# Kernel optimization log

Measured on AMD Instinct MI355X. Metric: run time of the kernel, lower is better.

The kernel has to match this reference:

```python
import jax, jax.numpy as jnp
import numpy as np

# Physics config (DPhysConfig defaults for the tracked robot)
MASS = 40.0        # robot mass [kg]
GRAV = 9.8         # gravity magnitude
STIFF = 1000.0     # terrain stiffness
DAMP = 100.0       # terrain damping
OMEGA_MAX = 2.0    # angular velocity clamp
DT = 0.01          # integration step [s]
LY = 0.6           # robot width (track separation)
RES = 0.1          # grid resolution [m/cell]


def skew(v):
    # v: (..., 3) -> (..., 3, 3)
    z = jnp.zeros_like(v[..., 0])
    return jnp.stack([
        jnp.stack([z, -v[..., 2], v[..., 1]], -1),
        jnp.stack([v[..., 2], z, -v[..., 0]], -1),
        jnp.stack([-v[..., 1], v[..., 0], z], -1)], -2)


def normalized(x, eps=1e-6):
    return x / jnp.clip(jnp.linalg.norm(x, axis=-1, keepdims=True), eps)


def bilinear(grid, xq, yq):
    # grid: (B, H, W) over [-H*RES/2, H*RES/2] x [-W*RES/2, W*RES/2]; xq, yq: (B, N)
    B, H, W = grid.shape
    u = jnp.clip((xq + H * RES / 2) / RES, 0.0, H - 1.001)
    v = jnp.clip((yq + W * RES / 2) / RES, 0.0, W - 1.001)
    u0 = jnp.floor(u).astype(jnp.int32)
    v0 = jnp.floor(v).astype(jnp.int32)
    du, dv = u - u0, v - v0
    b = jnp.arange(B)[:, None]
    g00 = grid[b, u0, v0]
    g10 = grid[b, u0 + 1, v0]
    g01 = grid[b, u0, v0 + 1]
    g11 = grid[b, u0 + 1, v0 + 1]
    return (g00 * (1 - du) * (1 - dv) + g10 * du * (1 - dv)
            + g01 * (1 - du) * dv + g11 * du * dv)


def inertia_inv(points, mass):
    # points: (N, 3) body-frame point masses -> inverse inertia (3, 3)
    mp = mass / points.shape[0]
    x, y, z = points[:, 0], points[:, 1], points[:, 2]
    Ixx = (mp * (y ** 2 + z ** 2)).sum()
    Iyy = (mp * (x ** 2 + z ** 2)).sum()
    Izz = (mp * (x ** 2 + y ** 2)).sum()
    Ixy = -(mp * x * y).sum()
    Ixz = -(mp * x * z).sum()
    Iyz = -(mp * y * z).sum()
    I = jnp.stack([jnp.stack([Ixx, Ixy, Ixz]),
                   jnp.stack([Ixy, Iyy, Iyz]),
                   jnp.stack([Ixz, Iyz, Izz])])
    return jnp.linalg.inv(I)


def _forward(z_grid, friction, controls, robot_points, x0, xd0, R0, omega0):
    dtype = z_grid.dtype
    I_inv = inertia_inv(robot_points, MASS)          # (3,3), joints fixed -> constant
    gx = jnp.gradient(z_grid, axis=1) / RES          # dz/dx on grid
    gy = jnp.gradient(z_grid, axis=2) / RES          # dz/dy on grid
    maskL = (robot_points[:, 1] < 0).astype(dtype)   # (N,) left track points
    maskR = 1.0 - maskL                              # right track points
    F_grav = MASS * GRAV * jnp.array([0.0, 0.0, -1.0], dtype=dtype)
    clamp = MASS * GRAV

    def dynamics(state, ctrl):
        x, xd, R, omega = state
        # world-frame body points: x_points @ R^T + x
        pts = jnp.einsum('nj,bkj->bnk', robot_points, R) + x[:, None]      # (B,N,3)
        xd_pts = xd[:, None] + jnp.cross(omega[:, None, :], pts - x[:, None], axis=-1)
        px, py = pts[..., 0], pts[..., 1]
        z = bilinear(z_grid, px, py)[..., None]                            # (B,N,1)
        nrm = normalized(jnp.stack([-bilinear(gx, px, py),
                                    -bilinear(gy, px, py),
                                    jnp.ones_like(px)], -1))               # (B,N,3)
        fr = bilinear(friction, px, py)[..., None]                         # (B,N,1)
        dh = pts[..., 2:3] - z
        in_c = jax.nn.sigmoid(-10.0 * dh)
        xd_n = jnp.sum(xd_pts * nrm, -1, keepdims=True)
        F_r = -(STIFF * dh + DAMP * xd_n) * nrm
        F_r = jnp.clip(F_r * in_c / jnp.sum(in_c, 1, keepdims=True), -clamp, clamp)
        thrust = normalized(R[..., 0])                                     # (B,3) first column
        Nmag = jnp.linalg.norm(F_r, axis=2)                                # (B,N)
        v, w = ctrl[:, 0], ctrl[:, 1]
        vL = (v - w * LY / 2)[:, None, None]
        vR = (v + w * LY / 2)[:, None, None]
        cmd = (maskL[None, :, None] * vL + maskR[None, :, None] * vR) * thrust[:, None, :]
        slip = fr * (cmd - xd_pts)
        slip_tau = slip - jnp.sum(slip * nrm, -1, keepdims=True) * nrm
        F_f = jnp.clip(Nmag[..., None] * slip_tau, -clamp, clamp)
        torque = jnp.sum(jnp.cross(pts - x[:, None], F_r + F_f, axis=-1), axis=1)
        omega_d = jnp.clip(torque @ I_inv.T, -OMEGA_MAX, OMEGA_MAX)
        xdd = (F_grav[None] + F_r.sum(1) + F_f.sum(1)) / MASS
        return xdd, omega_d

    def rot_step(R, omega, eps=1e-6):
        # Rodrigues' formula
        Ox = skew(omega)
        th = jnp.linalg.norm(omega, axis=-1)[:, None, None]
        Oxn = Ox / jnp.clip(th, eps)
        I3 = jnp.eye(3, dtype=R.dtype)
        return R @ (I3 + Oxn * jnp.sin(th * DT) + (Oxn @ Oxn) * (1 - jnp.cos(th * DT)))

    def step(state, ctrl):
        x, xd, R, omega = state
        xdd, omega_d = dynamics(state, ctrl)
        xd = xd + xdd * DT          # semi-implicit Euler, as in update_state
        x = x + xd * DT
        omega = omega + omega_d * DT
        R = rot_step(R, omega)
        return (x, xd, R, omega), x

    _, Xs = jax.lax.scan(step, (x0, xd0, R0, omega0), jnp.swapaxes(controls, 0, 1))
    return jnp.swapaxes(Xs, 0, 1)   # (B, T, 3) trajectory positions


def setup_inputs() -> dict:
    key = jax.random.key(0)
    ks = jax.random.split(key, 5)
    B, T, N, H, W = 64, 500, 128, 256, 256
    z_grid = jax.random.uniform(ks[0], (B, H, W), dtype=jnp.float32) * 0.2
    friction = jax.random.uniform(ks[1], (B, H, W), dtype=jnp.float32)
    controls = jax.random.normal(ks[2], (B, T, 2), dtype=jnp.float32) * jnp.array([1.0, 0.5], jnp.float32)
    robot_points = (jax.random.uniform(ks[3], (N, 3), dtype=jnp.float32) - 0.5) \
        * jnp.array([1.0, 0.6, 0.2], jnp.float32)
    x0 = jax.random.normal(ks[4], (B, 3), dtype=jnp.float32) * 0.1 + jnp.array([0.0, 0.0, 0.3], jnp.float32)
    xd0 = jnp.zeros((B, 3), jnp.float32)
    R0 = jnp.tile(jnp.eye(3, dtype=jnp.float32), (B, 1, 1))
    omega0 = jnp.zeros((B, 3), jnp.float32)
    return {"z_grid": z_grid, "friction": friction, "controls": controls,
            "robot_points": robot_points, "x0": x0, "xd0": xd0, "R0": R0, "omega0": omega0}


def reference(z_grid, friction, controls, robot_points, x0, xd0, R0, omega0):
    return _forward(z_grid, friction, controls, robot_points, x0, xd0, R0, omega0)
```

## Files before the change

kernel.cpp:

```cpp
#include <hip/hip_runtime.h>
#include <math.h>

#define GH 256
#define GW 256

typedef float f4 __attribute__((ext_vector_type(4), aligned(4)));
typedef float f2 __attribute__((ext_vector_type(2), aligned(4)));
typedef float f4l __attribute__((ext_vector_type(4)));

template<int CTRL, int RMASK>
__device__ __forceinline__ float dpp_add(float v) {
    int r = __builtin_amdgcn_update_dpp(0, __builtin_bit_cast(int, v), CTRL, RMASK, 0xF, true);
    return v + __builtin_bit_cast(float, r);
}
template<int CTRL, int RMASK>
__device__ __forceinline__ float dpp_max(float v) {
    int r = __builtin_amdgcn_update_dpp(0, __builtin_bit_cast(int, v), CTRL, RMASK, 0xF, true);
    return fmaxf(v, __builtin_bit_cast(float, r));
}

__device__ __forceinline__ float wave_sum63(float v) {
    v = dpp_add<0xB1, 0xF>(v);
    v = dpp_add<0x4E, 0xF>(v);
    v = dpp_add<0x141, 0xF>(v);
    v = dpp_add<0x140, 0xF>(v);
    v = dpp_add<0x142, 0xA>(v);
    v = dpp_add<0x143, 0xC>(v);
    return v;
}
__device__ __forceinline__ float wave_max63(float v) {
    v = dpp_max<0xB1, 0xF>(v);
    v = dpp_max<0x4E, 0xF>(v);
    v = dpp_max<0x141, 0xF>(v);
    v = dpp_max<0x140, 0xF>(v);
    v = dpp_max<0x142, 0xA>(v);
    v = dpp_max<0x143, 0xC>(v);
    return v;
}
__device__ __forceinline__ float rl63(float v) {
    return __builtin_bit_cast(float, __builtin_amdgcn_readlane(__builtin_bit_cast(int, v), 63));
}

__device__ __forceinline__ float frcp(float x)  { return __builtin_amdgcn_rcpf(x); }
__device__ __forceinline__ float frsq(float x)  { return __builtin_amdgcn_rsqf(x); }
__device__ __forceinline__ float fexp2(float x) { return __builtin_amdgcn_exp2f(x); }

__global__ __launch_bounds__(128) void dphys_kernel(
    const float* __restrict__ z_grid,
    const float* __restrict__ friction,
    const float* __restrict__ controls,
    const float* __restrict__ robot_points,
    const float* __restrict__ x0,
    const float* __restrict__ xd0,
    const float* __restrict__ R0,
    const float* __restrict__ omega0,
    float* __restrict__ out,
    int T)
{
    const int b = blockIdx.x;
    const int tid = threadIdx.x;
    const int wv = tid >> 6;
    __shared__ f4l ldsX[2][2][2];
    __shared__ f4l ldsY[2][2];

    const float* __restrict__ zg = z_grid + (size_t)b * (GH * GW);
    const float* __restrict__ fg = friction + (size_t)b * (GH * GW);
    const float* __restrict__ ct = controls + (size_t)b * (T * 2);
    float* __restrict__ ob = out + (size_t)b * (T * 3);

    const float ppx = robot_points[tid * 3 + 0];
    const float ppy = robot_points[tid * 3 + 1];
    const float ppz = robot_points[tid * 3 + 2];
    const bool isL = (ppy < 0.0f);

    float I6[6];
    I6[0] = ppy * ppy + ppz * ppz;
    I6[1] = ppx * ppx + ppz * ppz;
    I6[2] = ppx * ppx + ppy * ppy;
    I6[3] = ppx * ppy;
    I6[4] = ppx * ppz;
    I6[5] = ppy * ppz;
    #pragma unroll
    for (int k = 0; k < 6; ++k) I6[k] = rl63(wave_sum63(I6[k]));
    if ((tid & 63) == 63) {
        f4l t0; t0.x = I6[0]; t0.y = I6[1]; t0.z = I6[2]; t0.w = I6[3];
        f4l t1; t1.x = I6[4]; t1.y = I6[5]; t1.z = 0.f; t1.w = 0.f;
        ldsY[wv][0] = t0; ldsY[wv][1] = t1;
    }
    __syncthreads();
    {
        f4l o0 = ldsY[wv ^ 1][0], o1 = ldsY[wv ^ 1][1];
        I6[0] += o0.x; I6[1] += o0.y; I6[2] += o0.z;
        I6[3] += o0.w; I6[4] += o1.x; I6[5] += o1.y;
    }
    const float mp = 0.3125f;
    {
        double a = mp * I6[0], bb = mp * I6[1], c = mp * I6[2];
        double d = -(mp * I6[3]), e = -(mp * I6[4]), f = -(mp * I6[5]);
        double C00 = bb * c - f * f, C01 = e * f - d * c, C02 = d * f - bb * e;
        double C11 = a * c - e * e, C12 = d * e - a * f, C22 = a * bb - d * d;
        double idet = 1.0 / (a * C00 + d * C01 + e * C02);
        I6[0] = (float)(C00 * idet); I6[1] = (float)(C11 * idet); I6[2] = (float)(C22 * idet);
        I6[3] = (float)(C01 * idet); I6[4] = (float)(C02 * idet); I6[5] = (float)(C12 * idet);
    }
    const float i00 = I6[0], i11 = I6[1], i22 = I6[2];
    const float i01 = I6[3], i02 = I6[4], i12 = I6[5];

    float X0 = x0[b * 3 + 0], X1 = x0[b * 3 + 1], X2 = x0[b * 3 + 2];
    float V0 = xd0[b * 3 + 0], V1 = xd0[b * 3 + 1], V2 = xd0[b * 3 + 2];
    float W0 = omega0[b * 3 + 0], W1 = omega0[b * 3 + 1], W2 = omega0[b * 3 + 2];
    float R00 = R0[b * 9 + 0], R01 = R0[b * 9 + 1], R02 = R0[b * 9 + 2];
    float R10 = R0[b * 9 + 3], R11 = R0[b * 9 + 4], R12 = R0[b * 9 + 5];
    float R20 = R0[b * 9 + 6], R21 = R0[b * 9 + 7], R22 = R0[b * 9 + 8];

    for (int t = 0; t < T; ++t) {
        const int par = t & 1;
        f2 cc = *(const f2*)(ct + t * 2);

        float rx = R00 * ppx + R01 * ppy + R02 * ppz;
        float ry = R10 * ppx + R11 * ppy + R12 * ppz;
        float rz = R20 * ppx + R21 * ppy + R22 * ppz;
        float Px = rx + X0, Py = ry + X1, Pz = rz + X2;
        float l0 = Px - X0, l1 = Py - X1, l2 = Pz - X2;
        float u = (Px + 12.8f) * 10.0f;
        u = fminf(fmaxf(u, 0.0f), 254.999f);
        float vvq = (Py + 12.8f) * 10.0f;
        vvq = fminf(fmaxf(vvq, 0.0f), 254.999f);
        int u0 = (int)u, v0 = (int)vvq;
        bool interior = (u0 >= 1) & (u0 <= 253) & (v0 >= 1) & (v0 <= 253);
        bool fast = __all(interior);

        float zz, fr, gxs, gys;
        float du = u - (float)u0, dv = vvq - (float)v0;
        float w00 = (1.0f - du) * (1.0f - dv);
        float w10 = du * (1.0f - dv);
        float w01 = (1.0f - du) * dv;
        float w11 = du * dv;

        float cv = cc.x, cw = cc.y;
        float half = (cw * 0.6f) * 0.5f;
        float vLs = cv - half, vRs = cv + half;
        float rtn = frsq(R00 * R00 + R10 * R10 + R20 * R20);
        float th0 = R00 * rtn, th1 = R10 * rtn, th2 = R20 * rtn;
        float xp0 = V0 + (W1 * l2 - W2 * l1);
        float xp1 = V1 + (W2 * l0 - W0 * l2);
        float xp2 = V2 + (W0 * l1 - W1 * l0);
        float cmd = isL ? vLs : vRs;
        float ct0 = cmd * th0 - xp0;
        float ct1 = cmd * th1 - xp1;
        float ct2 = cmd * th2 - xp2;

        if (fast) {
            int base = (u0 - 1) * GW + (v0 - 1);
            f4 P0 = *(const f4*)(zg + base);
            f4 P1 = *(const f4*)(zg + base + GW);
            f4 P2 = *(const f4*)(zg + base + 2 * GW);
            f4 P3 = *(const f4*)(zg + base + 3 * GW);
            int fb = u0 * GW + v0;
            f2 F0 = *(const f2*)(fg + fb);
            f2 F1 = *(const f2*)(fg + fb + GW);
            zz = P1.y * w00 + P2.y * w10 + P1.z * w01 + P2.z * w11;
            fr = F0.x * w00 + F1.x * w10 + F0.y * w01 + F1.y * w11;
            float gx00 = (P2.y - P0.y) * 5.0f;
            float gx10 = (P3.y - P1.y) * 5.0f;
            float gx01 = (P2.z - P0.z) * 5.0f;
            float gx11 = (P3.z - P1.z) * 5.0f;
            float gy00 = (P1.z - P1.x) * 5.0f;
            float gy10 = (P2.z - P2.x) * 5.0f;
            float gy01 = (P1.w - P1.y) * 5.0f;
            float gy11 = (P2.w - P2.y) * 5.0f;
            gxs = gx00 * w00 + gx10 * w10 + gx01 * w01 + gx11 * w11;
            gys = gy00 * w00 + gy10 * w10 + gy01 * w01 + gy11 * w11;
        } else {
            int basei = u0 * GW + v0;
            zz = zg[basei] * w00 + zg[basei + GW] * w10 + zg[basei + 1] * w01 + zg[basei + GW + 1] * w11;
            fr = fg[basei] * w00 + fg[basei + GW] * w10 + fg[basei + 1] * w01 + fg[basei + GW + 1] * w11;
            float gx[2][2], gy[2][2];
            #pragma unroll
            for (int ii = 0; ii < 2; ++ii) {
                int i = u0 + ii;
                int ipu = (i < GH - 1) ? i + 1 : i;
                int imu = (i > 0) ? i - 1 : i;
                float scu = (ipu - imu == 2) ? 0.5f : 1.0f;
                #pragma unroll
                for (int jj = 0; jj < 2; ++jj) {
                    int j = v0 + jj;
                    int jpv = (j < GW - 1) ? j + 1 : j;
                    int jmv = (j > 0) ? j - 1 : j;
                    float scv = (jpv - jmv == 2) ? 0.5f : 1.0f;
                    gx[ii][jj] = ((zg[ipu * GW + j] - zg[imu * GW + j]) * scu) * 10.0f;
                    gy[ii][jj] = ((zg[i * GW + jpv] - zg[i * GW + jmv]) * scv) * 10.0f;
                }
            }
            gxs = gx[0][0] * w00 + gx[1][0] * w10 + gx[0][1] * w01 + gx[1][1] * w11;
            gys = gy[0][0] * w00 + gy[1][0] * w10 + gy[0][1] * w01 + gy[1][1] * w11;
        }

        float rn = frsq(gxs * gxs + gys * gys + 1.0f);
        float nx = -gxs * rn, ny = -gys * rn, nzc = rn;
        float dh = Pz - zz;
        float ex = fexp2(dh * 14.426950408889634f);
        float ic = frcp(1.0f + ex);
        float xdn = xp0 * nx + xp1 * ny + xp2 * nzc;

        float mag = -(1000.0f * dh + 100.0f * xdn);
        float mic = mag * ic;
        float m_abs = fabsf(mic);
        float sl0 = fr * ct0, sl1 = fr * ct1, sl2 = fr * ct2;
        float sdn = sl0 * nx + sl1 * ny + sl2 * nzc;
        float st0 = sl0 - sdn * nx;
        float st1 = sl1 - sdn * ny;
        float st2 = sl2 - sdn * nzc;
        float g0 = mic * nx  + m_abs * st0;
        float g1 = mic * ny  + m_abs * st1;
        float g2 = mic * nzc + m_abs * st2;
        float q0 = l1 * g2 - l2 * g1;
        float q1 = l2 * g0 - l0 * g2;
        float q2 = l0 * g1 - l1 * g0;
        float stm = fmaxf(fmaxf(fabsf(st0), fabsf(st1)), fabsf(st2));
        float worst = fmaxf(stm, 1.0f) * m_abs;

        float d_ic = wave_sum63(ic);
        float d_g0 = wave_sum63(g0), d_g1 = wave_sum63(g1), d_g2 = wave_sum63(g2);
        float d_q0 = wave_sum63(q0), d_q1 = wave_sum63(q1), d_q2 = wave_sum63(q2);
        float d_rw = wave_max63(worst);
        if ((tid & 63) == 63) {
            f4l h0; h0.x = d_g0; h0.y = d_g1; h0.z = d_g2; h0.w = d_q0;
            f4l h1; h1.x = d_q1; h1.y = d_q2; h1.z = d_ic; h1.w = d_rw;
            ldsX[par][wv][0] = h0; ldsX[par][wv][1] = h1;
        }
        float o_ic = rl63(d_ic);
        float o_g0 = rl63(d_g0), o_g1 = rl63(d_g1), o_g2 = rl63(d_g2);
        float o_q0 = rl63(d_q0), o_q1 = rl63(d_q1), o_q2 = rl63(d_q2);
        float o_rw = rl63(d_rw);
        __syncthreads();
        f4l e0 = ldsX[par][wv ^ 1][0], e1 = ldsX[par][wv ^ 1][1];
        float sic = o_ic + e1.z;
        float rwm = fmaxf(o_rw, e1.w);
        float rsic = frcp(sic);

        float FT0, FT1, FT2, TQ0, TQ1, TQ2;
        if (rwm <= 391.0f * sic) {
            FT0 = (o_g0 + e0.x) * rsic;
            FT1 = (o_g1 + e0.y) * rsic;
            FT2 = (o_g2 + e0.z) * rsic;
            TQ0 = (o_q0 + e0.w) * rsic;
            TQ1 = (o_q1 + e1.x) * rsic;
            TQ2 = (o_q2 + e1.y) * rsic;
        } else {
            float s = mic * rsic;
            float Fr0 = fminf(fmaxf(s * nx,  -392.0f), 392.0f);
            float Fr1 = fminf(fmaxf(s * ny,  -392.0f), 392.0f);
            float Fr2 = fminf(fmaxf(s * nzc, -392.0f), 392.0f);
            float Nm = __builtin_amdgcn_sqrtf(Fr0 * Fr0 + Fr1 * Fr1 + Fr2 * Fr2);
            float Ff0 = fminf(fmaxf(Nm * st0, -392.0f), 392.0f);
            float Ff1 = fminf(fmaxf(Nm * st1, -392.0f), 392.0f);
            float Ff2 = fminf(fmaxf(Nm * st2, -392.0f), 392.0f);
            float S0 = Fr0 + Ff0, S1 = Fr1 + Ff1, S2 = Fr2 + Ff2;
            float U0 = l1 * S2 - l2 * S1;
            float U1 = l2 * S0 - l0 * S2;
            float U2 = l0 * S1 - l1 * S0;
            float dS0 = wave_sum63(S0), dS1 = wave_sum63(S1), dS2 = wave_sum63(S2);
            float dU0 = wave_sum63(U0), dU1 = wave_sum63(U1), dU2 = wave_sum63(U2);
            if ((tid & 63) == 63) {
                f4l h0; h0.x = dS0; h0.y = dS1; h0.z = dS2; h0.w = dU0;
                f4l h1; h1.x = dU1; h1.y = dU2; h1.z = 0.f; h1.w = 0.f;
                ldsY[wv][0] = h0; ldsY[wv][1] = h1;
            }
            __syncthreads();
            f4l c0 = ldsY[wv ^ 1][0], c1 = ldsY[wv ^ 1][1];
            FT0 = rl63(dS0) + c0.x; FT1 = rl63(dS1) + c0.y; FT2 = rl63(dS2) + c0.z;
            TQ0 = rl63(dU0) + c0.w; TQ1 = rl63(dU1) + c1.x; TQ2 = rl63(dU2) + c1.y;
        }

        float od0 = fminf(fmaxf(TQ0 * i00 + TQ1 * i01 + TQ2 * i02, -2.0f), 2.0f);
        float od1 = fminf(fmaxf(TQ0 * i01 + TQ1 * i11 + TQ2 * i12, -2.0f), 2.0f);
        float od2 = fminf(fmaxf(TQ0 * i02 + TQ1 * i12 + TQ2 * i22, -2.0f), 2.0f);

        V0 += (FT0 * 0.025f) * 0.01f;
        V1 += (FT1 * 0.025f) * 0.01f;
        V2 += ((-392.0f + FT2) * 0.025f) * 0.01f;
        X0 += V0 * 0.01f; X1 += V1 * 0.01f; X2 += V2 * 0.01f;
        W0 += od0 * 0.01f; W1 += od1 * 0.01f; W2 += od2 * 0.01f;

        if (tid == 0) {
            ob[t * 3 + 0] = X0;
            ob[t * 3 + 1] = X1;
            ob[t * 3 + 2] = X2;
        }

        float th2s = W0 * W0 + W1 * W1 + W2 * W2;
        float a2 = th2s * 1e-4f;
        float s1 = 0.01f - a2 * (0.01f / 6.0f);
        float c2 = 5e-5f - a2 * (1e-4f / 24.0f);
        float w01p = W0 * W1, w02p = W0 * W2, w12p = W1 * W2;
        float A00 = 1.0f - c2 * (W1 * W1 + W2 * W2);
        float A11 = 1.0f - c2 * (W0 * W0 + W2 * W2);
        float A22 = 1.0f - c2 * (W0 * W0 + W1 * W1);
        float A01 = c2 * w01p - s1 * W2;
        float A10 = c2 * w01p + s1 * W2;
        float A02 = c2 * w02p + s1 * W1;
        float A20 = c2 * w02p - s1 * W1;
        float A12 = c2 * w12p - s1 * W0;
        float A21 = c2 * w12p + s1 * W0;
        float N00 = R00 * A00 + R01 * A10 + R02 * A20;
        float N01 = R00 * A01 + R01 * A11 + R02 * A21;
        float N02 = R00 * A02 + R01 * A12 + R02 * A22;
        float N10 = R10 * A00 + R11 * A10 + R12 * A20;
        float N11 = R10 * A01 + R11 * A11 + R12 * A21;
        float N12 = R10 * A02 + R11 * A12 + R12 * A22;
        float N20 = R20 * A00 + R21 * A10 + R22 * A20;
        float N21 = R20 * A01 + R21 * A11 + R22 * A21;
        float N22 = R20 * A02 + R21 * A12 + R22 * A22;
        R00 = N00; R01 = N01; R02 = N02;
        R10 = N10; R11 = N11; R12 = N12;
        R20 = N20; R21 = N21; R22 = N22;
    }
}

extern "C" void kernel_launch(void* const* d_in, const int* in_sizes, int n_in,
                              void* d_out, int out_size, void* d_ws, size_t ws_size,
                              hipStream_t stream) {
    const float* z_grid       = (const float*)d_in[0];
    const float* friction     = (const float*)d_in[1];
    const float* controls     = (const float*)d_in[2];
    const float* robot_points = (const float*)d_in[3];
    const float* x0           = (const float*)d_in[4];
    const float* xd0          = (const float*)d_in[5];
    const float* R0           = (const float*)d_in[6];
    const float* omega0       = (const float*)d_in[7];
    int B = in_sizes[4] / 3;
    int T = in_sizes[2] / (B * 2);
    dphys_kernel<<<B, 128, 0, stream>>>(z_grid, friction, controls, robot_points,
                                        x0, xd0, R0, omega0, (float*)d_out, T);
}
```

Before: 554.9 us.

## Precompute interleaved height/gradient/friction texture in workspace for single-gather bilinear lookups

Adds a prep kernel that writes a float4 per grid cell holding height, x/y gradients and friction into the workspace. The main simulation kernel then does four float4 gathers and one vector bilinear blend per step, replacing separate height and friction loads, on-the-fly gradient stencils and the interior/boundary branch. The loop is also unrolled by two. This costs an extra launch and about 67 MB of workspace writes and reads, and the old kernel remains as a fallback when the workspace is too small.

```diff
diff --git a/kernel.cpp b/kernel.cpp
--- a/kernel.cpp
+++ b/kernel.cpp
@@ -18,7 +18,6 @@
     int r = __builtin_amdgcn_update_dpp(0, __builtin_bit_cast(int, v), CTRL, RMASK, 0xF, true);
     return fmaxf(v, __builtin_bit_cast(float, r));
 }
-
 __device__ __forceinline__ float wave_sum63(float v) {
     v = dpp_add<0xB1, 0xF>(v);
     v = dpp_add<0x4E, 0xF>(v);
@@ -40,12 +39,266 @@
 __device__ __forceinline__ float rl63(float v) {
     return __builtin_bit_cast(float, __builtin_amdgcn_readlane(__builtin_bit_cast(int, v), 63));
 }
-
 __device__ __forceinline__ float frcp(float x)  { return __builtin_amdgcn_rcpf(x); }
 __device__ __forceinline__ float frsq(float x)  { return __builtin_amdgcn_rsqf(x); }
 __device__ __forceinline__ float fexp2(float x) { return __builtin_amdgcn_exp2f(x); }
 
+__global__ __launch_bounds__(256) void prep_kernel(
+    const float* __restrict__ z_grid,
+    const float* __restrict__ friction,
+    f4* __restrict__ tex)
+{
+    const int j = threadIdx.x;
+    const int i = blockIdx.x;
+    const int b = blockIdx.y;
+    const float* __restrict__ z = z_grid + (size_t)b * (GH * GW);
+    int ipu = (i < GH - 1) ? i + 1 : i;
+    int imu = (i > 0) ? i - 1 : i;
+    int jpv = (j < GW - 1) ? j + 1 : j;
+    int jmv = (j > 0) ? j - 1 : j;
+    float scu = (ipu - imu == 2) ? 0.5f : 1.0f;
+    float scv = (jpv - jmv == 2) ? 0.5f : 1.0f;
+    float gx = ((z[ipu * GW + j] - z[imu * GW + j]) * scu) * 10.0f;
+    float gy = ((z[i * GW + jpv] - z[i * GW + jmv]) * scv) * 10.0f;
+    f4 o;
+    o.x = z[i * GW + j];
+    o.y = gx;
+    o.z = gy;
+    o.w = friction[(size_t)b * (GH * GW) + i * GW + j];
+    tex[(size_t)b * (GH * GW) + i * GW + j] = o;
+}
+
 __global__ __launch_bounds__(128) void dphys_kernel(
+    const f4* __restrict__ tex,
+    const float* __restrict__ controls,
+    const float* __restrict__ robot_points,
+    const float* __restrict__ x0,
+    const float* __restrict__ xd0,
+    const float* __restrict__ R0,
+    const float* __restrict__ omega0,
+    float* __restrict__ out,
+    int T)
+{
+    const int b = blockIdx.x;
+    const int tid = threadIdx.x;
+    const int wv = tid >> 6;
+    __shared__ f4l ldsX[2][2][2];
+    __shared__ f4l ldsY[2][2];
+
+    const f4* __restrict__ tb = tex + (size_t)b * (GH * GW);
+    const float* __restrict__ ct = controls + (size_t)b * (T * 2);
+    float* __restrict__ ob = out + (size_t)b * (T * 3);
+
+    const float ppx = robot_points[tid * 3 + 0];
+    const float ppy = robot_points[tid * 3 + 1];
+    const float ppz = robot_points[tid * 3 + 2];
+    const bool isL = (ppy < 0.0f);
+
+    float I6[6];
+    I6[0] = ppy * ppy + ppz * ppz;
+    I6[1] = ppx * ppx + ppz * ppz;
+    I6[2] = ppx * ppx + ppy * ppy;
+    I6[3] = ppx * ppy;
+    I6[4] = ppx * ppz;
+    I6[5] = ppy * ppz;
+    #pragma unroll
+    for (int k = 0; k < 6; ++k) I6[k] = rl63(wave_sum63(I6[k]));
+    if ((tid & 63) == 63) {
+        f4l t0; t0.x = I6[0]; t0.y = I6[1]; t0.z = I6[2]; t0.w = I6[3];
+        f4l t1; t1.x = I6[4]; t1.y = I6[5]; t1.z = 0.f; t1.w = 0.f;
+        ldsY[wv][0] = t0; ldsY[wv][1] = t1;
+    }
+    __syncthreads();
+    {
+        f4l o0 = ldsY[wv ^ 1][0], o1 = ldsY[wv ^ 1][1];
+        I6[0] += o0.x; I6[1] += o0.y; I6[2] += o0.z;
+        I6[3] += o0.w; I6[4] += o1.x; I6[5] += o1.y;
+    }
+    const float mp = 0.3125f;
+    {
+        double a = mp * I6[0], bb = mp * I6[1], c = mp * I6[2];
+        double d = -(mp * I6[3]), e = -(mp * I6[4]), f = -(mp * I6[5]);
+        double C00 = bb * c - f * f, C01 = e * f - d * c, C02 = d * f - bb * e;
+        double C11 = a * c - e * e, C12 = d * e - a * f, C22 = a * bb - d * d;
+        double idet = 1.0 / (a * C00 + d * C01 + e * C02);
+        I6[0] = (float)(C00 * idet); I6[1] = (float)(C11 * idet); I6[2] = (float)(C22 * idet);
+        I6[3] = (float)(C01 * idet); I6[4] = (float)(C02 * idet); I6[5] = (float)(C12 * idet);
+    }
+    const float i00 = I6[0], i11 = I6[1], i22 = I6[2];
+    const float i01 = I6[3], i02 = I6[4], i12 = I6[5];
+
+    float X0 = x0[b * 3 + 0], X1 = x0[b * 3 + 1], X2 = x0[b * 3 + 2];
+    float V0 = xd0[b * 3 + 0], V1 = xd0[b * 3 + 1], V2 = xd0[b * 3 + 2];
+    float W0 = omega0[b * 3 + 0], W1 = omega0[b * 3 + 1], W2 = omega0[b * 3 + 2];
+    float R00 = R0[b * 9 + 0], R01 = R0[b * 9 + 1], R02 = R0[b * 9 + 2];
+    float R10 = R0[b * 9 + 3], R11 = R0[b * 9 + 4], R12 = R0[b * 9 + 5];
+    float R20 = R0[b * 9 + 6], R21 = R0[b * 9 + 7], R22 = R0[b * 9 + 8];
+
+    #pragma unroll 2
+    for (int t = 0; t < T; ++t) {
+        const int par = t & 1;
+        f2 cc = *(const f2*)(ct + t * 2);
+
+        float rx = R00 * ppx + R01 * ppy + R02 * ppz;
+        float ry = R10 * ppx + R11 * ppy + R12 * ppz;
+        float rz = R20 * ppx + R21 * ppy + R22 * ppz;
+        float Px = rx + X0, Py = ry + X1, Pz = rz + X2;
+        float l0 = Px - X0, l1 = Py - X1, l2 = Pz - X2;
+        float u = (Px + 12.8f) * 10.0f;
+        u = fminf(fmaxf(u, 0.0f), 254.999f);
+        float vvq = (Py + 12.8f) * 10.0f;
+        vvq = fminf(fmaxf(vvq, 0.0f), 254.999f);
+        int u0 = (int)u, v0 = (int)vvq;
+        int idx = (u0 << 8) + v0;
+        f4 c00 = tb[idx];
+        f4 c01 = tb[idx + 1];
+        f4 c10 = tb[idx + GW];
+        f4 c11 = tb[idx + GW + 1];
+
+        float du = u - (float)u0, dv = vvq - (float)v0;
+        float w00 = (1.0f - du) * (1.0f - dv);
+        float w10 = du * (1.0f - dv);
+        float w01 = (1.0f - du) * dv;
+        float w11 = du * dv;
+        float cv = cc.x, cw = cc.y;
+        float half = (cw * 0.6f) * 0.5f;
+        float vLs = cv - half, vRs = cv + half;
+        float rtn = frsq(R00 * R00 + R10 * R10 + R20 * R20);
+        float th0 = R00 * rtn, th1 = R10 * rtn, th2 = R20 * rtn;
+        float xp0 = V0 + (W1 * l2 - W2 * l1);
+        float xp1 = V1 + (W2 * l0 - W0 * l2);
+        float xp2 = V2 + (W0 * l1 - W1 * l0);
+        float cmd = isL ? vLs : vRs;
+        float ct0 = cmd * th0 - xp0;
+        float ct1 = cmd * th1 - xp1;
+        float ct2 = cmd * th2 - xp2;
+
+        f4 cb = c00 * w00 + c10 * w10 + c01 * w01 + c11 * w11;
+        float zz = cb.x, gxs = cb.y, gys = cb.z, fr = cb.w;
+
+        float rn = frsq(gxs * gxs + gys * gys + 1.0f);
+        float nx = -gxs * rn, ny = -gys * rn, nzc = rn;
+        float dh = Pz - zz;
+        float ex = fexp2(dh * 14.426950408889634f);
+        float ic = frcp(1.0f + ex);
+        float xdn = xp0 * nx + xp1 * ny + xp2 * nzc;
+
+        float mag = -(1000.0f * dh + 100.0f * xdn);
+        float mic = mag * ic;
+        float m_abs = fabsf(mic);
+        float sl0 = fr * ct0, sl1 = fr * ct1, sl2 = fr * ct2;
+        float sdn = sl0 * nx + sl1 * ny + sl2 * nzc;
+        float st0 = sl0 - sdn * nx;
+        float st1 = sl1 - sdn * ny;
+        float st2 = sl2 - sdn * nzc;
+        float g0 = mic * nx  + m_abs * st0;
+        float g1 = mic * ny  + m_abs * st1;
+        float g2 = mic * nzc + m_abs * st2;
+        float q0 = l1 * g2 - l2 * g1;
+        float q1 = l2 * g0 - l0 * g2;
+        float q2 = l0 * g1 - l1 * g0;
+        float stm = fmaxf(fmaxf(fabsf(st0), fabsf(st1)), fabsf(st2));
+        float worst = fmaxf(stm, 1.0f) * m_abs;
+
+        float d_ic = wave_sum63(ic);
+        float d_g0 = wave_sum63(g0), d_g1 = wave_sum63(g1), d_g2 = wave_sum63(g2);
+        float d_q0 = wave_sum63(q0), d_q1 = wave_sum63(q1), d_q2 = wave_sum63(q2);
+        float d_rw = wave_max63(worst);
+        if ((tid & 63) == 63) {
+            f4l h0; h0.x = d_g0; h0.y = d_g1; h0.z = d_g2; h0.w = d_q0;
+            f4l h1; h1.x = d_q1; h1.y = d_q2; h1.z = d_ic; h1.w = d_rw;
+            ldsX[par][wv][0] = h0; ldsX[par][wv][1] = h1;
+        }
+        float o_ic = rl63(d_ic);
+        float o_g0 = rl63(d_g0), o_g1 = rl63(d_g1), o_g2 = rl63(d_g2);
+        float o_q0 = rl63(d_q0), o_q1 = rl63(d_q1), o_q2 = rl63(d_q2);
+        float o_rw = rl63(d_rw);
+        __syncthreads();
+        f4l e0 = ldsX[par][wv ^ 1][0], e1 = ldsX[par][wv ^ 1][1];
+        float sic = o_ic + e1.z;
+        float rwm = fmaxf(o_rw, e1.w);
+        float rsic = frcp(sic);
+
+        float FT0, FT1, FT2, TQ0, TQ1, TQ2;
+        if (rwm <= 391.0f * sic) {
+            FT0 = (o_g0 + e0.x) * rsic;
+            FT1 = (o_g1 + e0.y) * rsic;
+            FT2 = (o_g2 + e0.z) * rsic;
+            TQ0 = (o_q0 + e0.w) * rsic;
+            TQ1 = (o_q1 + e1.x) * rsic;
+            TQ2 = (o_q2 + e1.y) * rsic;
+        } else {
+            float s = mic * rsic;
+            float Fr0 = fminf(fmaxf(s * nx,  -392.0f), 392.0f);
+            float Fr1 = fminf(fmaxf(s * ny,  -392.0f), 392.0f);
+            float Fr2 = fminf(fmaxf(s * nzc, -392.0f), 392.0f);
+            float Nm = __builtin_amdgcn_sqrtf(Fr0 * Fr0 + Fr1 * Fr1 + Fr2 * Fr2);
+            float Ff0 = fminf(fmaxf(Nm * st0, -392.0f), 392.0f);
+            float Ff1 = fminf(fmaxf(Nm * st1, -392.0f), 392.0f);
+            float Ff2 = fminf(fmaxf(Nm * st2, -392.0f), 392.0f);
+            float S0 = Fr0 + Ff0, S1 = Fr1 + Ff1, S2 = Fr2 + Ff2;
+            float U0 = l1 * S2 - l2 * S1;
+            float U1 = l2 * S0 - l0 * S2;
+            float U2 = l0 * S1 - l1 * S0;
+            float dS0 = wave_sum63(S0), dS1 = wave_sum63(S1), dS2 = wave_sum63(S2);
+            float dU0 = wave_sum63(U0), dU1 = wave_sum63(U1), dU2 = wave_sum63(U2);
+            if ((tid & 63) == 63) {
+                f4l h0; h0.x = dS0; h0.y = dS1; h0.z = dS2; h0.w = dU0;
+                f4l h1; h1.x = dU1; h1.y = dU2; h1.z = 0.f; h1.w = 0.f;
+                ldsY[wv][0] = h0; ldsY[wv][1] = h1;
+            }
+            __syncthreads();
+            f4l c0 = ldsY[wv ^ 1][0], c1 = ldsY[wv ^ 1][1];
+            FT0 = rl63(dS0) + c0.x; FT1 = rl63(dS1) + c0.y; FT2 = rl63(dS2) + c0.z;
+            TQ0 = rl63(dU0) + c0.w; TQ1 = rl63(dU1) + c1.x; TQ2 = rl63(dU2) + c1.y;
+        }
+
+        float od0 = fminf(fmaxf(TQ0 * i00 + TQ1 * i01 + TQ2 * i02, -2.0f), 2.0f);
+        float od1 = fminf(fmaxf(TQ0 * i01 + TQ1 * i11 + TQ2 * i12, -2.0f), 2.0f);
+        float od2 = fminf(fmaxf(TQ0 * i02 + TQ1 * i12 + TQ2 * i22, -2.0f), 2.0f);
+
+        V0 += (FT0 * 0.025f) * 0.01f;
+        V1 += (FT1 * 0.025f) * 0.01f;
+        V2 += ((-392.0f + FT2) * 0.025f) * 0.01f;
+        X0 += V0 * 0.01f; X1 += V1 * 0.01f; X2 += V2 * 0.01f;
+        W0 += od0 * 0.01f; W1 += od1 * 0.01f; W2 += od2 * 0.01f;
+
+        if (tid == 0) {
+            ob[t * 3 + 0] = X0;
+            ob[t * 3 + 1] = X1;
+            ob[t * 3 + 2] = X2;
+        }
+
+        float th2s = W0 * W0 + W1 * W1 + W2 * W2;
+        float a2 = th2s * 1e-4f;
+        float s1 = 0.01f - a2 * (0.01f / 6.0f);
+        float c2 = 5e-5f - a2 * (1e-4f / 24.0f);
+        float w01p = W0 * W1, w02p = W0 * W2, w12p = W1 * W2;
+        float A00 = 1.0f - c2 * (W1 * W1 + W2 * W2);
+        float A11 = 1.0f - c2 * (W0 * W0 + W2 * W2);
+        float A22 = 1.0f - c2 * (W0 * W0 + W1 * W1);
+        float A01 = c2 * w01p - s1 * W2;
+        float A10 = c2 * w01p + s1 * W2;
+        float A02 = c2 * w02p + s1 * W1;
+        float A20 = c2 * w02p - s1 * W1;
+        float A12 = c2 * w12p - s1 * W0;
+        float A21 = c2 * w12p + s1 * W0;
+        float N00 = R00 * A00 + R01 * A10 + R02 * A20;
+        float N01 = R00 * A01 + R01 * A11 + R02 * A21;
+        float N02 = R00 * A02 + R01 * A12 + R02 * A22;
+        float N10 = R10 * A00 + R11 * A10 + R12 * A20;
+        float N11 = R10 * A01 + R11 * A11 + R12 * A21;
+        float N12 = R10 * A02 + R11 * A12 + R12 * A22;
+        float N20 = R20 * A00 + R21 * A10 + R22 * A20;
+        float N21 = R20 * A01 + R21 * A11 + R22 * A21;
+        float N22 = R20 * A02 + R21 * A12 + R22 * A22;
+        R00 = N00; R01 = N01; R02 = N02;
+        R10 = N10; R11 = N11; R12 = N12;
+        R20 = N20; R21 = N21; R22 = N22;
+    }
+}
+
+__global__ __launch_bounds__(128) void dphys_kernel_fb(
     const float* __restrict__ z_grid,
     const float* __restrict__ friction,
     const float* __restrict__ controls,
@@ -116,7 +369,6 @@
     for (int t = 0; t < T; ++t) {
         const int par = t & 1;
         f2 cc = *(const f2*)(ct + t * 2);
-
         float rx = R00 * ppx + R01 * ppy + R02 * ppz;
         float ry = R10 * ppx + R11 * ppy + R12 * ppz;
         float rz = R20 * ppx + R21 * ppy + R22 * ppz;
@@ -128,7 +380,7 @@
         vvq = fminf(fmaxf(vvq, 0.0f), 254.999f);
         int u0 = (int)u, v0 = (int)vvq;
         bool interior = (u0 >= 1) & (u0 <= 253) & (v0 >= 1) & (v0 <= 253);
-        bool fast = __all(interior);
+        bool fastp = __all(interior);
 
         float zz, fr, gxs, gys;
         float du = u - (float)u0, dv = vvq - (float)v0;
@@ -150,7 +402,7 @@
         float ct1 = cmd * th1 - xp1;
         float ct2 = cmd * th2 - xp2;
 
-        if (fast) {
+        if (fastp) {
             int base = (u0 - 1) * GW + (v0 - 1);
             f4 P0 = *(const f4*)(zg + base);
             f4 P1 = *(const f4*)(zg + base + GW);
@@ -331,6 +583,13 @@
     const float* omega0       = (const float*)d_in[7];
     int B = in_sizes[4] / 3;
     int T = in_sizes[2] / (B * 2);
-    dphys_kernel<<<B, 128, 0, stream>>>(z_grid, friction, controls, robot_points,
-                                        x0, xd0, R0, omega0, (float*)d_out, T);
-}
+    size_t need = (size_t)B * GH * GW * sizeof(float) * 4;
+    if (ws_size >= need) {
+        prep_kernel<<<dim3(GH, B), GW, 0, stream>>>(z_grid, friction, (f4*)d_ws);
+        dphys_kernel<<<B, 128, 0, stream>>>((const f4*)d_ws, controls, robot_points,
+                                            x0, xd0, R0, omega0, (float*)d_out, T);
+    } else {
+        dphys_kernel_fb<<<B, 128, 0, stream>>>(z_grid, friction, controls, robot_points,
+                                               x0, xd0, R0, omega0, (float*)d_out, T);
+    }
+}
```

Result: faster. 479.9 us (-13.5%).

## Precompute interleaved height/gradient/friction texture and simulate two batches per block

Applied to the files above, without the earlier changes.

Adds a prep kernel that packs height, the central-difference gradients and friction into one float4 per cell in the workspace. The main kernel then does four float4 gathers per point per step and handles two batch elements per 128-thread block, using paired f2 arithmetic so the two serial step chains interleave. This targets per-step gather latency and the latency-bound serial loop. In exchange it adds a full-grid preprocessing pass, 64 MB of workspace traffic, and halves the number of blocks. The old kernel is kept as a fallback when the workspace is too small.

```diff
diff --git a/kernel.cpp b/kernel.cpp
--- a/kernel.cpp
+++ b/kernel.cpp
@@ -18,7 +18,6 @@
     int r = __builtin_amdgcn_update_dpp(0, __builtin_bit_cast(int, v), CTRL, RMASK, 0xF, true);
     return fmaxf(v, __builtin_bit_cast(float, r));
 }
-
 __device__ __forceinline__ float wave_sum63(float v) {
     v = dpp_add<0xB1, 0xF>(v);
     v = dpp_add<0x4E, 0xF>(v);
@@ -40,12 +39,338 @@
 __device__ __forceinline__ float rl63(float v) {
     return __builtin_bit_cast(float, __builtin_amdgcn_readlane(__builtin_bit_cast(int, v), 63));
 }
-
 __device__ __forceinline__ float frcp(float x)  { return __builtin_amdgcn_rcpf(x); }
 __device__ __forceinline__ float frsq(float x)  { return __builtin_amdgcn_rsqf(x); }
 __device__ __forceinline__ float fexp2(float x) { return __builtin_amdgcn_exp2f(x); }
 
-__global__ __launch_bounds__(128) void dphys_kernel(
+__device__ __forceinline__ f2 pabs(f2 a)        { f2 r; r.x = fabsf(a.x); r.y = fabsf(a.y); return r; }
+__device__ __forceinline__ f2 pmaxv(f2 a, f2 b) { f2 r; r.x = fmaxf(a.x, b.x); r.y = fmaxf(a.y, b.y); return r; }
+__device__ __forceinline__ f2 pclamp(f2 a, float lo, float hi) {
+    f2 r; r.x = fminf(fmaxf(a.x, lo), hi); r.y = fminf(fmaxf(a.y, lo), hi); return r;
+}
+__device__ __forceinline__ f2 prsq(f2 a) { f2 r; r.x = frsq(a.x); r.y = frsq(a.y); return r; }
+
+__global__ __launch_bounds__(256) void prep_kernel(
+    const float* __restrict__ z_grid,
+    const float* __restrict__ friction,
+    f4* __restrict__ tex)
+{
+    const int j = threadIdx.x;
+    const int i = blockIdx.x;
+    const int b = blockIdx.y;
+    const float* __restrict__ z = z_grid + (size_t)b * (GH * GW);
+    int ipu = (i < GH - 1) ? i + 1 : i;
+    int imu = (i > 0) ? i - 1 : i;
+    int jpv = (j < GW - 1) ? j + 1 : j;
+    int jmv = (j > 0) ? j - 1 : j;
+    float scu = (ipu - imu == 2) ? 0.5f : 1.0f;
+    float scv = (jpv - jmv == 2) ? 0.5f : 1.0f;
+    float gx = ((z[ipu * GW + j] - z[imu * GW + j]) * scu) * 10.0f;
+    float gy = ((z[i * GW + jpv] - z[i * GW + jmv]) * scv) * 10.0f;
+    f4 o;
+    o.x = z[i * GW + j];
+    o.y = gx;
+    o.z = gy;
+    o.w = friction[(size_t)b * (GH * GW) + i * GW + j];
+    tex[(size_t)b * (GH * GW) + i * GW + j] = o;
+}
+
+__global__ __launch_bounds__(128, 1) void dphys_kernel2p(
+    const f4* __restrict__ tex,
+    const float* __restrict__ controls,
+    const float* __restrict__ robot_points,
+    const float* __restrict__ x0,
+    const float* __restrict__ xd0,
+    const float* __restrict__ R0,
+    const float* __restrict__ omega0,
+    float* __restrict__ out,
+    int T, int B)
+{
+    const int tid = threadIdx.x;
+    const int wv = tid >> 6;
+    __shared__ f4l ldsX[2][2][2][2];
+    __shared__ f4l ldsY[2][2][2];
+
+    int bA = blockIdx.x * 2;
+    int bB = bA + 1; if (bB >= B) bB = B - 1;
+
+    const f4* __restrict__ tbA = tex + (size_t)bA * (GH * GW);
+    const f4* __restrict__ tbB = tex + (size_t)bB * (GH * GW);
+    const float* __restrict__ ctA = controls + (size_t)bA * (T * 2);
+    const float* __restrict__ ctB = controls + (size_t)bB * (T * 2);
+    float* __restrict__ obA = out + (size_t)bA * (T * 3);
+    float* __restrict__ obB = out + (size_t)bB * (T * 3);
+
+    const float ppx = robot_points[tid * 3 + 0];
+    const float ppy = robot_points[tid * 3 + 1];
+    const float ppz = robot_points[tid * 3 + 2];
+    const bool isL = (ppy < 0.0f);
+
+    float I6[6];
+    I6[0] = ppy * ppy + ppz * ppz;
+    I6[1] = ppx * ppx + ppz * ppz;
+    I6[2] = ppx * ppx + ppy * ppy;
+    I6[3] = ppx * ppy;
+    I6[4] = ppx * ppz;
+    I6[5] = ppy * ppz;
+    #pragma unroll
+    for (int k = 0; k < 6; ++k) I6[k] = rl63(wave_sum63(I6[k]));
+    if ((tid & 63) == 63) {
+        f4l t0; t0.x = I6[0]; t0.y = I6[1]; t0.z = I6[2]; t0.w = I6[3];
+        f4l t1; t1.x = I6[4]; t1.y = I6[5]; t1.z = 0.f; t1.w = 0.f;
+        ldsY[0][wv][0] = t0; ldsY[0][wv][1] = t1;
+    }
+    __syncthreads();
+    {
+        f4l o0 = ldsY[0][wv ^ 1][0], o1 = ldsY[0][wv ^ 1][1];
+        I6[0] += o0.x; I6[1] += o0.y; I6[2] += o0.z;
+        I6[3] += o0.w; I6[4] += o1.x; I6[5] += o1.y;
+    }
+    const float mp = 0.3125f;
+    {
+        double a = mp * I6[0], bb = mp * I6[1], c = mp * I6[2];
+        double d = -(mp * I6[3]), e = -(mp * I6[4]), f = -(mp * I6[5]);
+        double C00 = bb * c - f * f, C01 = e * f - d * c, C02 = d * f - bb * e;
+        double C11 = a * c - e * e, C12 = d * e - a * f, C22 = a * bb - d * d;
+        double idet = 1.0 / (a * C00 + d * C01 + e * C02);
+        I6[0] = (float)(C00 * idet); I6[1] = (float)(C11 * idet); I6[2] = (float)(C22 * idet);
+        I6[3] = (float)(C01 * idet); I6[4] = (float)(C02 * idet); I6[5] = (float)(C12 * idet);
+    }
+    const float i00 = I6[0], i11 = I6[1], i22 = I6[2];
+    const float i01 = I6[3], i02 = I6[4], i12 = I6[5];
+
+    f2 X0, X1, X2, V0, V1, V2, W0, W1, W2;
+    f2 R00, R01, R02, R10, R11, R12, R20, R21, R22;
+    X0.x = x0[bA*3+0]; X0.y = x0[bB*3+0];
+    X1.x = x0[bA*3+1]; X1.y = x0[bB*3+1];
+    X2.x = x0[bA*3+2]; X2.y = x0[bB*3+2];
+    V0.x = xd0[bA*3+0]; V0.y = xd0[bB*3+0];
+    V1.x = xd0[bA*3+1]; V1.y = xd0[bB*3+1];
+    V2.x = xd0[bA*3+2]; V2.y = xd0[bB*3+2];
+    W0.x = omega0[bA*3+0]; W0.y = omega0[bB*3+0];
+    W1.x = omega0[bA*3+1]; W1.y = omega0[bB*3+1];
+    W2.x = omega0[bA*3+2]; W2.y = omega0[bB*3+2];
+    R00.x = R0[bA*9+0]; R00.y = R0[bB*9+0];
+    R01.x = R0[bA*9+1]; R01.y = R0[bB*9+1];
+    R02.x = R0[bA*9+2]; R02.y = R0[bB*9+2];
+    R10.x = R0[bA*9+3]; R10.y = R0[bB*9+3];
+    R11.x = R0[bA*9+4]; R11.y = R0[bB*9+4];
+    R12.x = R0[bA*9+5]; R12.y = R0[bB*9+5];
+    R20.x = R0[bA*9+6]; R20.y = R0[bB*9+6];
+    R21.x = R0[bA*9+7]; R21.y = R0[bB*9+7];
+    R22.x = R0[bA*9+8]; R22.y = R0[bB*9+8];
+
+    for (int t = 0; t < T; ++t) {
+        const int par = t & 1;
+        f2 ccA = *(const f2*)(ctA + t * 2);
+        f2 ccB = *(const f2*)(ctB + t * 2);
+        f2 cv; cv.x = ccA.x; cv.y = ccB.x;
+        f2 cw; cw.x = ccA.y; cw.y = ccB.y;
+
+        f2 rx = R00 * ppx + R01 * ppy + R02 * ppz;
+        f2 ry = R10 * ppx + R11 * ppy + R12 * ppz;
+        f2 rz = R20 * ppx + R21 * ppy + R22 * ppz;
+        f2 Px = rx + X0, Py = ry + X1, Pz = rz + X2;
+        f2 l0 = Px - X0, l1 = Py - X1, l2 = Pz - X2;
+        f2 u = pclamp((Px + 12.8f) * 10.0f, 0.0f, 254.999f);
+        f2 vq = pclamp((Py + 12.8f) * 10.0f, 0.0f, 254.999f);
+        int u0A = (int)u.x, u0B = (int)u.y;
+        int v0A = (int)vq.x, v0B = (int)vq.y;
+        f2 du; du.x = u.x - (float)u0A; du.y = u.y - (float)u0B;
+        f2 dv; dv.x = vq.x - (float)v0A; dv.y = vq.y - (float)v0B;
+        int idxA = (u0A << 8) + v0A;
+        int idxB = (u0B << 8) + v0B;
+        f4 a00 = tbA[idxA], a01 = tbA[idxA + 1], a10 = tbA[idxA + GW], a11 = tbA[idxA + GW + 1];
+        f4 b00 = tbB[idxB], b01 = tbB[idxB + 1], b10 = tbB[idxB + GW], b11 = tbB[idxB + GW + 1];
+
+        f2 half_ = (cw * 0.6f) * 0.5f;
+        f2 vLs = cv - half_, vRs = cv + half_;
+        f2 rtn = prsq(R00 * R00 + R10 * R10 + R20 * R20);
+        f2 th0 = R00 * rtn, th1 = R10 * rtn, th2 = R20 * rtn;
+        f2 xp0 = V0 + (W1 * l2 - W2 * l1);
+        f2 xp1 = V1 + (W2 * l0 - W0 * l2);
+        f2 xp2 = V2 + (W0 * l1 - W1 * l0);
+        f2 cmd = isL ? vLs : vRs;
+        f2 ct0 = cmd * th0 - xp0;
+        f2 ct1 = cmd * th1 - xp1;
+        f2 ct2 = cmd * th2 - xp2;
+
+        float w00A = (1.0f - du.x) * (1.0f - dv.x);
+        float w10A = du.x * (1.0f - dv.x);
+        float w01A = (1.0f - du.x) * dv.x;
+        float w11A = du.x * dv.x;
+        float w00B = (1.0f - du.y) * (1.0f - dv.y);
+        float w10B = du.y * (1.0f - dv.y);
+        float w01B = (1.0f - du.y) * dv.y;
+        float w11B = du.y * dv.y;
+        f4 cbA = a00 * w00A + a10 * w10A + a01 * w01A + a11 * w11A;
+        f4 cbB = b00 * w00B + b10 * w10B + b01 * w01B + b11 * w11B;
+        f2 zz;  zz.x = cbA.x;  zz.y = cbB.x;
+        f2 gxs; gxs.x = cbA.y; gxs.y = cbB.y;
+        f2 gys; gys.x = cbA.z; gys.y = cbB.z;
+        f2 fr;  fr.x = cbA.w;  fr.y = cbB.w;
+
+        f2 rn = prsq(gxs * gxs + gys * gys + 1.0f);
+        f2 nx = -gxs * rn, ny = -gys * rn, nz = rn;
+        f2 dh = Pz - zz;
+        f2 ex; ex.x = fexp2(dh.x * 14.426950408889634f); ex.y = fexp2(dh.y * 14.426950408889634f);
+        f2 ic; ic.x = frcp(1.0f + ex.x); ic.y = frcp(1.0f + ex.y);
+        f2 xdn = xp0 * nx + xp1 * ny + xp2 * nz;
+
+        f2 mag = -(1000.0f * dh + 100.0f * xdn);
+        f2 mic = mag * ic;
+        f2 m_abs = pabs(mic);
+        f2 sl0 = fr * ct0, sl1 = fr * ct1, sl2 = fr * ct2;
+        f2 sdn = sl0 * nx + sl1 * ny + sl2 * nz;
+        f2 st0 = sl0 - sdn * nx;
+        f2 st1 = sl1 - sdn * ny;
+        f2 st2 = sl2 - sdn * nz;
+        f2 g0 = mic * nx + m_abs * st0;
+        f2 g1 = mic * ny + m_abs * st1;
+        f2 g2 = mic * nz + m_abs * st2;
+        f2 q0 = l1 * g2 - l2 * g1;
+        f2 q1 = l2 * g0 - l0 * g2;
+        f2 q2 = l0 * g1 - l1 * g0;
+        f2 stm = pmaxv(pmaxv(pabs(st0), pabs(st1)), pabs(st2));
+        f2 one; one.x = 1.0f; one.y = 1.0f;
+        f2 worst = pmaxv(stm, one) * m_abs;
+
+        float d_icA = wave_sum63(ic.x), d_icB = wave_sum63(ic.y);
+        float d_g0A = wave_sum63(g0.x), d_g0B = wave_sum63(g0.y);
+        float d_g1A = wave_sum63(g1.x), d_g1B = wave_sum63(g1.y);
+        float d_g2A = wave_sum63(g2.x), d_g2B = wave_sum63(g2.y);
+        float d_q0A = wave_sum63(q0.x), d_q0B = wave_sum63(q0.y);
+        float d_q1A = wave_sum63(q1.x), d_q1B = wave_sum63(q1.y);
+        float d_q2A = wave_sum63(q2.x), d_q2B = wave_sum63(q2.y);
+        float d_rwA = wave_max63(worst.x), d_rwB = wave_max63(worst.y);
+        if ((tid & 63) == 63) {
+            f4l h0; h0.x = d_g0A; h0.y = d_g1A; h0.z = d_g2A; h0.w = d_q0A;
+            f4l h1; h1.x = d_q1A; h1.y = d_q2A; h1.z = d_icA; h1.w = d_rwA;
+            ldsX[par][0][wv][0] = h0; ldsX[par][0][wv][1] = h1;
+            f4l h2; h2.x = d_g0B; h2.y = d_g1B; h2.z = d_g2B; h2.w = d_q0B;
+            f4l h3; h3.x = d_q1B; h3.y = d_q2B; h3.z = d_icB; h3.w = d_rwB;
+            ldsX[par][1][wv][0] = h2; ldsX[par][1][wv][1] = h3;
+        }
+        float o_icA = rl63(d_icA), o_icB = rl63(d_icB);
+        float o_g0A = rl63(d_g0A), o_g0B = rl63(d_g0B);
+        float o_g1A = rl63(d_g1A), o_g1B = rl63(d_g1B);
+        float o_g2A = rl63(d_g2A), o_g2B = rl63(d_g2B);
+        float o_q0A = rl63(d_q0A), o_q0B = rl63(d_q0B);
+        float o_q1A = rl63(d_q1A), o_q1B = rl63(d_q1B);
+        float o_q2A = rl63(d_q2A), o_q2B = rl63(d_q2B);
+        float o_rwA = rl63(d_rwA), o_rwB = rl63(d_rwB);
+        __syncthreads();
+
+        f4l e0A = ldsX[par][0][wv ^ 1][0], e1A = ldsX[par][0][wv ^ 1][1];
+        f4l e0B = ldsX[par][1][wv ^ 1][0], e1B = ldsX[par][1][wv ^ 1][1];
+        float sicA = o_icA + e1A.z, sicB = o_icB + e1B.z;
+        float rwmA = fmaxf(o_rwA, e1A.w), rwmB = fmaxf(o_rwB, e1B.w);
+        float rsicA = frcp(sicA), rsicB = frcp(sicB);
+
+        f2 FT0, FT1, FT2, TQ0, TQ1, TQ2;
+        FT0.x = (o_g0A + e0A.x) * rsicA; FT0.y = (o_g0B + e0B.x) * rsicB;
+        FT1.x = (o_g1A + e0A.y) * rsicA; FT1.y = (o_g1B + e0B.y) * rsicB;
+        FT2.x = (o_g2A + e0A.z) * rsicA; FT2.y = (o_g2B + e0B.z) * rsicB;
+        TQ0.x = (o_q0A + e0A.w) * rsicA; TQ0.y = (o_q0B + e0B.w) * rsicB;
+        TQ1.x = (o_q1A + e1A.x) * rsicA; TQ1.y = (o_q1B + e1B.x) * rsicB;
+        TQ2.x = (o_q2A + e1A.y) * rsicA; TQ2.y = (o_q2B + e1B.y) * rsicB;
+
+        if (rwmA > 391.0f * sicA) {
+            float s = mic.x * rsicA;
+            float Fr0 = fminf(fmaxf(s * nx.x, -392.0f), 392.0f);
+            float Fr1 = fminf(fmaxf(s * ny.x, -392.0f), 392.0f);
+            float Fr2 = fminf(fmaxf(s * nz.x, -392.0f), 392.0f);
+            float Nm = __builtin_amdgcn_sqrtf(Fr0 * Fr0 + Fr1 * Fr1 + Fr2 * Fr2);
+            float Ff0 = fminf(fmaxf(Nm * st0.x, -392.0f), 392.0f);
+            float Ff1 = fminf(fmaxf(Nm * st1.x, -392.0f), 392.0f);
+            float Ff2 = fminf(fmaxf(Nm * st2.x, -392.0f), 392.0f);
+            float S0 = Fr0 + Ff0, S1 = Fr1 + Ff1, S2 = Fr2 + Ff2;
+            float U0 = l1.x * S2 - l2.x * S1;
+            float U1 = l2.x * S0 - l0.x * S2;
+            float U2 = l0.x * S1 - l1.x * S0;
+            float dS0 = wave_sum63(S0), dS1 = wave_sum63(S1), dS2 = wave_sum63(S2);
+            float dU0 = wave_sum63(U0), dU1 = wave_sum63(U1), dU2 = wave_sum63(U2);
+            if ((tid & 63) == 63) {
+                f4l h0; h0.x = dS0; h0.y = dS1; h0.z = dS2; h0.w = dU0;
+                f4l h1; h1.x = dU1; h1.y = dU2; h1.z = 0.f; h1.w = 0.f;
+                ldsY[0][wv][0] = h0; ldsY[0][wv][1] = h1;
+            }
+            __syncthreads();
+            f4l c0 = ldsY[0][wv ^ 1][0], c1 = ldsY[0][wv ^ 1][1];
+            FT0.x = rl63(dS0) + c0.x; FT1.x = rl63(dS1) + c0.y; FT2.x = rl63(dS2) + c0.z;
+            TQ0.x = rl63(dU0) + c0.w; TQ1.x = rl63(dU1) + c1.x; TQ2.x = rl63(dU2) + c1.y;
+        }
+        if (rwmB > 391.0f * sicB) {
+            float s = mic.y * rsicB;
+            float Fr0 = fminf(fmaxf(s * nx.y, -392.0f), 392.0f);
+            float Fr1 = fminf(fmaxf(s * ny.y, -392.0f), 392.0f);
+            float Fr2 = fminf(fmaxf(s * nz.y, -392.0f), 392.0f);
+            float Nm = __builtin_amdgcn_sqrtf(Fr0 * Fr0 + Fr1 * Fr1 + Fr2 * Fr2);
+            float Ff0 = fminf(fmaxf(Nm * st0.y, -392.0f), 392.0f);
+            float Ff1 = fminf(fmaxf(Nm * st1.y, -392.0f), 392.0f);
+            float Ff2 = fminf(fmaxf(Nm * st2.y, -392.0f), 392.0f);
+            float S0 = Fr0 + Ff0, S1 = Fr1 + Ff1, S2 = Fr2 + Ff2;
+            float U0 = l1.y * S2 - l2.y * S1;
+            float U1 = l2.y * S0 - l0.y * S2;
+            float U2 = l0.y * S1 - l1.y * S0;
+            float dS0 = wave_sum63(S0), dS1 = wave_sum63(S1), dS2 = wave_sum63(S2);
+            float dU0 = wave_sum63(U0), dU1 = wave_sum63(U1), dU2 = wave_sum63(U2);
+            if ((tid & 63) == 63) {
+                f4l h0; h0.x = dS0; h0.y = dS1; h0.z = dS2; h0.w = dU0;
+                f4l h1; h1.x = dU1; h1.y = dU2; h1.z = 0.f; h1.w = 0.f;
+                ldsY[1][wv][0] = h0; ldsY[1][wv][1] = h1;
+            }
+            __syncthreads();
+            f4l c0 = ldsY[1][wv ^ 1][0], c1 = ldsY[1][wv ^ 1][1];
+            FT0.y = rl63(dS0) + c0.x; FT1.y = rl63(dS1) + c0.y; FT2.y = rl63(dS2) + c0.z;
+            TQ0.y = rl63(dU0) + c0.w; TQ1.y = rl63(dU1) + c1.x; TQ2.y = rl63(dU2) + c1.y;
+        }
+
+        f2 od0 = pclamp(TQ0 * i00 + TQ1 * i01 + TQ2 * i02, -2.0f, 2.0f);
+        f2 od1 = pclamp(TQ0 * i01 + TQ1 * i11 + TQ2 * i12, -2.0f, 2.0f);
+        f2 od2 = pclamp(TQ0 * i02 + TQ1 * i12 + TQ2 * i22, -2.0f, 2.0f);
+
+        V0 += (FT0 * 0.025f) * 0.01f;
+        V1 += (FT1 * 0.025f) * 0.01f;
+        V2 += ((FT2 - 392.0f) * 0.025f) * 0.01f;
+        X0 += V0 * 0.01f; X1 += V1 * 0.01f; X2 += V2 * 0.01f;
+        W0 += od0 * 0.01f; W1 += od1 * 0.01f; W2 += od2 * 0.01f;
+
+        if (tid == 0) {
+            obA[t * 3 + 0] = X0.x; obA[t * 3 + 1] = X1.x; obA[t * 3 + 2] = X2.x;
+            obB[t * 3 + 0] = X0.y; obB[t * 3 + 1] = X1.y; obB[t * 3 + 2] = X2.y;
+        }
+
+        f2 th2s = W0 * W0 + W1 * W1 + W2 * W2;
+        f2 a2 = th2s * 1e-4f;
+        f2 s1 = 0.01f - a2 * (0.01f / 6.0f);
+        f2 c2 = 5e-5f - a2 * (1e-4f / 24.0f);
+        f2 w01p = W0 * W1, w02p = W0 * W2, w12p = W1 * W2;
+        f2 A00 = 1.0f - c2 * (W1 * W1 + W2 * W2);
+        f2 A11 = 1.0f - c2 * (W0 * W0 + W2 * W2);
+        f2 A22 = 1.0f - c2 * (W0 * W0 + W1 * W1);
+        f2 A01 = c2 * w01p - s1 * W2;
+        f2 A10 = c2 * w01p + s1 * W2;
+        f2 A02 = c2 * w02p + s1 * W1;
+        f2 A20 = c2 * w02p - s1 * W1;
+        f2 A12 = c2 * w12p - s1 * W0;
+        f2 A21 = c2 * w12p + s1 * W0;
+        f2 N00 = R00 * A00 + R01 * A10 + R02 * A20;
+        f2 N01 = R00 * A01 + R01 * A11 + R02 * A21;
+        f2 N02 = R00 * A02 + R01 * A12 + R02 * A22;
+        f2 N10 = R10 * A00 + R11 * A10 + R12 * A20;
+        f2 N11 = R10 * A01 + R11 * A11 + R12 * A21;
+        f2 N12 = R10 * A02 + R11 * A12 + R12 * A22;
+        f2 N20 = R20 * A00 + R21 * A10 + R22 * A20;
+        f2 N21 = R20 * A01 + R21 * A11 + R22 * A21;
+        f2 N22 = R20 * A02 + R21 * A12 + R22 * A22;
+        R00 = N00; R01 = N01; R02 = N02;
+        R10 = N10; R11 = N11; R12 = N12;
+        R20 = N20; R21 = N21; R22 = N22;
+    }
+}
+
+__global__ __launch_bounds__(128) void dphys_kernel_fb(
     const float* __restrict__ z_grid,
     const float* __restrict__ friction,
     const float* __restrict__ controls,
@@ -116,7 +441,6 @@
     for (int t = 0; t < T; ++t) {
         const int par = t & 1;
         f2 cc = *(const f2*)(ct + t * 2);
-
         float rx = R00 * ppx + R01 * ppy + R02 * ppz;
         float ry = R10 * ppx + R11 * ppy + R12 * ppz;
         float rz = R20 * ppx + R21 * ppy + R22 * ppz;
@@ -128,7 +452,7 @@
         vvq = fminf(fmaxf(vvq, 0.0f), 254.999f);
         int u0 = (int)u, v0 = (int)vvq;
         bool interior = (u0 >= 1) & (u0 <= 253) & (v0 >= 1) & (v0 <= 253);
-        bool fast = __all(interior);
+        bool fastp = __all(interior);
 
         float zz, fr, gxs, gys;
         float du = u - (float)u0, dv = vvq - (float)v0;
@@ -150,7 +474,7 @@
         float ct1 = cmd * th1 - xp1;
         float ct2 = cmd * th2 - xp2;
 
-        if (fast) {
+        if (fastp) {
             int base = (u0 - 1) * GW + (v0 - 1);
             f4 P0 = *(const f4*)(zg + base);
             f4 P1 = *(const f4*)(zg + base + GW);
@@ -331,6 +655,14 @@
     const float* omega0       = (const float*)d_in[7];
     int B = in_sizes[4] / 3;
     int T = in_sizes[2] / (B * 2);
-    dphys_kernel<<<B, 128, 0, stream>>>(z_grid, friction, controls, robot_points,
-                                        x0, xd0, R0, omega0, (float*)d_out, T);
-}
+    size_t need = (size_t)B * GH * GW * sizeof(float) * 4;
+    if (ws_size >= need) {
+        prep_kernel<<<dim3(GH, B), GW, 0, stream>>>(z_grid, friction, (f4*)d_ws);
+        int nb = (B + 1) / 2;
+        dphys_kernel2p<<<nb, 128, 0, stream>>>((const f4*)d_ws, controls, robot_points,
+                                               x0, xd0, R0, omega0, (float*)d_out, T, B);
+    } else {
+        dphys_kernel_fb<<<B, 128, 0, stream>>>(z_grid, friction, controls, robot_points,
+                                               x0, xd0, R0, omega0, (float*)d_out, T);
+    }
+}
```

Result: slower. 728.7 us (+31.3%).
